# Optimization experiments

Hardware: AMD Instinct MI355X
Metric: run time of the kernel (lower is better)

## Reference

```python
import jax, jax.numpy as jnp
import numpy as np

NUM_PITCHES = 88
H_FEAT = 188
LSTM_UNITS = 48
N_STATES = 5
CTX_HID = 16
CTX_OUT = 4


def _glorot(key, shape):
    fan_in, fan_out = shape[1], shape[0]
    lim = (6.0 / (fan_in + fan_out)) ** 0.5
    return jax.random.uniform(key, shape, jnp.float32, -lim, lim)


def setup_inputs() -> dict:
    key = jax.random.key(0)
    ks = jax.random.split(key, 16)
    B, T = 16, 256
    pitch_features = jax.random.normal(ks[0], (B, NUM_PITCHES, H_FEAT, T), jnp.float32)
    prev_context = jax.random.uniform(ks[1], (B, NUM_PITCHES, 3), jnp.float32)
    # context net params
    fc1_w = _glorot(ks[2], (CTX_HID, 3)); fc1_b = jnp.zeros((CTX_HID,), jnp.float32)
    fc2_w = _glorot(ks[3], (CTX_HID, CTX_HID)); fc2_b = jnp.zeros((CTX_HID,), jnp.float32)
    fc3_w = _glorot(ks[4], (CTX_OUT, CTX_HID)); fc3_b = jnp.zeros((CTX_OUT,), jnp.float32)
    # lstm1: input H_FEAT+4 -> 48; gates order i,f,g,o (torch convention)
    in1 = H_FEAT + CTX_OUT
    lstm1_wih = _glorot(ks[5], (4 * LSTM_UNITS, in1))
    lstm1_whh = _glorot(ks[6], (4 * LSTM_UNITS, LSTM_UNITS))
    lstm1_bih = jnp.zeros((4 * LSTM_UNITS,), jnp.float32)
    lstm1_bhh = jnp.zeros((4 * LSTM_UNITS,), jnp.float32)
    lstm2_wih = _glorot(ks[7], (4 * LSTM_UNITS, LSTM_UNITS))
    lstm2_whh = _glorot(ks[8], (4 * LSTM_UNITS, LSTM_UNITS))
    lstm2_bih = jnp.zeros((4 * LSTM_UNITS,), jnp.float32)
    lstm2_bhh = jnp.zeros((4 * LSTM_UNITS,), jnp.float32)
    fc_states_w = _glorot(ks[9], (N_STATES, LSTM_UNITS))
    fc_states_b = jnp.zeros((N_STATES,), jnp.float32)
    return dict(pitch_features=pitch_features, prev_context=prev_context,
                fc1_w=fc1_w, fc1_b=fc1_b, fc2_w=fc2_w, fc2_b=fc2_b,
                fc3_w=fc3_w, fc3_b=fc3_b,
                lstm1_wih=lstm1_wih, lstm1_whh=lstm1_whh, lstm1_bih=lstm1_bih, lstm1_bhh=lstm1_bhh,
                lstm2_wih=lstm2_wih, lstm2_whh=lstm2_whh, lstm2_bih=lstm2_bih, lstm2_bhh=lstm2_bhh,
                fc_states_w=fc_states_w, fc_states_b=fc_states_b)


def _lstm_scan(x, wih, whh, bih, bhh):
    # x: (S, N, In); zero init state; returns (S, N, U)
    S, N, _ = x.shape
    U = whh.shape[1]
    xg = jnp.einsum('sni,gi->sng', x, wih) + bih + bhh  # precompute input gates

    def step(carry, xg_t):
        h, c = carry
        g = xg_t + h @ whh.T  # (N, 4U)
        i, f, gg, o = jnp.split(g, 4, axis=-1)
        c = jax.nn.sigmoid(f) * c + jax.nn.sigmoid(i) * jnp.tanh(gg)
        h = jax.nn.sigmoid(o) * jnp.tanh(c)
        return (h, c), h

    init = (jnp.zeros((N, U), x.dtype), jnp.zeros((N, U), x.dtype))
    _, hs = jax.lax.scan(step, init, xg)
    return hs


def reference(pitch_features, prev_context,
              fc1_w, fc1_b, fc2_w, fc2_b, fc3_w, fc3_b,
              lstm1_wih, lstm1_whh, lstm1_bih, lstm1_bhh,
              lstm2_wih, lstm2_whh, lstm2_bih, lstm2_bhh,
              fc_states_w, fc_states_b):
    B, P, H, T = pitch_features.shape
    # Context net (context never updates across t in the original loop)
    x = jax.nn.relu(prev_context @ fc1_w.T + fc1_b)
    x = jax.nn.relu(x @ fc2_w.T + fc2_b)
    ctx_emb = x @ fc3_w.T + fc3_b  # (B, P, 4)
    # Each timestep t is independent: LSTM runs over the pitch axis (len 88)
    # with zero initial state every step. Fold (B, T) into batch N.
    pf = jnp.transpose(pitch_features, (1, 0, 3, 2)).reshape(P, B * T, H)  # (P, BT, H)
    ce = jnp.broadcast_to(ctx_emb[:, None, :, :], (B, T, P, CTX_OUT))
    ce = jnp.transpose(ce, (2, 0, 1, 3)).reshape(P, B * T, CTX_OUT)
    seq = jnp.concatenate([pf, ce], axis=-1)  # (P, BT, H+4)
    h = _lstm_scan(seq, lstm1_wih, lstm1_whh, lstm1_bih, lstm1_bhh)
    h = _lstm_scan(h, lstm2_wih, lstm2_whh, lstm2_bih, lstm2_bhh)
    logits = h @ fc_states_w.T + fc_states_b  # (P, BT, 5)
    logits = logits.reshape(P, B, T, N_STATES)
    logits = jnp.transpose(logits, (1, 0, 3, 2))  # (B, P, 5, T)
    return jax.nn.softmax(logits, axis=2)
```

## Files before the change

### kernel.cpp

```cpp
#include <hip/hip_runtime.h>
#include <hip/hip_bf16.h>
#include <cstdint>

#define P_ 88
#define B_ 16
#define T_ 256
#define H_ 188
#define G_ 192
#define U_ 48
#define N_ 4096

typedef __attribute__((ext_vector_type(8))) short bf16x8;
typedef __attribute__((ext_vector_type(8))) _Float16 f16x8;
typedef __attribute__((ext_vector_type(4))) float f32x4;

__device__ __forceinline__ float sigf(float x) {
  return __builtin_amdgcn_rcpf(1.0f + __expf(-x));
}
__device__ __forceinline__ float tanh_f(float x) {
  return 1.0f - 2.0f * __builtin_amdgcn_rcpf(1.0f + __expf(2.0f * x));
}
__device__ __forceinline__ unsigned short f2bs(float v) {
  union { __hip_bfloat16 h; unsigned short s; } u;
  u.h = __float2bfloat16(v);
  return u.s;
}
__device__ __forceinline__ float bs2f(unsigned short s) {
  union { unsigned int u; float f; } x;
  x.u = ((unsigned int)s) << 16;
  return x.f;
}
__device__ __forceinline__ float hs2f(unsigned short s) {
  union { unsigned short u; _Float16 h; } x;
  x.u = s;
  return (float)x.h;
}
__device__ __forceinline__ unsigned short f2hs(float v) {
  union { _Float16 h; unsigned short s; } x;
  x.h = (_Float16)v;
  return x.s;
}

__device__ __forceinline__ void lds_barrier() {
  asm volatile("s_waitcnt lgkmcnt(0)\n\ts_barrier" ::: "memory");
}

__global__ void ctx_kernel(const float* __restrict__ pc,
                           const float* __restrict__ fc1w, const float* __restrict__ fc1b,
                           const float* __restrict__ fc2w, const float* __restrict__ fc2b,
                           const float* __restrict__ fc3w, const float* __restrict__ fc3b,
                           const float* __restrict__ wih1,
                           const float* __restrict__ bih1, const float* __restrict__ bhh1,
                           float* __restrict__ ctxg) {
  int bp = blockIdx.x * 64 + threadIdx.x;
  if (bp >= B_ * P_) return;
  float p0 = pc[bp * 3 + 0], p1 = pc[bp * 3 + 1], p2 = pc[bp * 3 + 2];
  float x1[16], x2[16];
#pragma unroll
  for (int jj = 0; jj < 16; ++jj)
    x1[jj] = fmaxf(0.f, fc1w[jj * 3 + 0] * p0 + fc1w[jj * 3 + 1] * p1 + fc1w[jj * 3 + 2] * p2 + fc1b[jj]);
#pragma unroll
  for (int jj = 0; jj < 16; ++jj) {
    float s = fc2b[jj];
#pragma unroll
    for (int i = 0; i < 16; ++i) s += fc2w[jj * 16 + i] * x1[i];
    x2[jj] = fmaxf(0.f, s);
  }
  float ce[4];
#pragma unroll
  for (int jj = 0; jj < 4; ++jj) {
    float s = fc3b[jj];
#pragma unroll
    for (int i = 0; i < 16; ++i) s += fc3w[jj * 16 + i] * x2[i];
    ce[jj] = s;
  }
  float* op = ctxg + (size_t)bp * G_;
  for (int g = 0; g < G_; ++g) {
    const float* wr = wih1 + (size_t)g * G_ + H_;
    op[g] = bih1[g] + bhh1[g] + ce[0] * wr[0] + ce[1] * wr[1] + ce[2] * wr[2] + ce[3] * wr[3];
  }
}

__global__ __launch_bounds__(256) void wfrag_kernel(const float* __restrict__ wih1,
                                                    f16x8* __restrict__ wfrag) {
  const int idx = blockIdx.x * 256 + threadIdx.x;
  if (idx >= 12 * 6 * 64) return;
  const int l = idx & 63;
  const int kc = (idx >> 6) % 6;
  const int j = idx / 384;
  const int g = j * 16 + (l & 15);
  const int k0 = kc * 32 + (l >> 4) * 8;
  f16x8 v;
#pragma unroll
  for (int e = 0; e < 8; ++e) {
    const int k = k0 + e;
    const float wv = (k < H_) ? wih1[(size_t)g * G_ + k] : 0.f;
    v[e] = (_Float16)wv;
  }
  wfrag[idx] = v;
}

__global__ __launch_bounds__(256, 3) void gemm_mfma(const float* __restrict__ pf,
                                                    const f16x8* __restrict__ wfrag,
                                                    const float* __restrict__ ctxg,
                                                    unsigned short* __restrict__ xg2) {
  const int bp = blockIdx.x >> 1, tb = blockIdx.x & 1;
  const int p = bp % P_, b = bp / P_;
  const int tid = threadIdx.x;
  const int w = tid >> 6, l = tid & 63;
  const int lj = l & 15, lq = l >> 4;

  __shared__ __align__(16) char ldsraw[49152];
  _Float16(*Ahi)[34] = (_Float16(*)[34])ldsraw;
  _Float16(*Alo)[34] = (_Float16(*)[34])(ldsraw + 8704);

  float cg[12];
#pragma unroll
  for (int jn = 0; jn < 12; ++jn)
    cg[jn] = ctxg[(size_t)bp * G_ + jn * 16 + lj];

  f32x4 acc[2][12];
#pragma unroll
  for (int mt = 0; mt < 2; ++mt)
#pragma unroll
    for (int jn = 0; jn < 12; ++jn)
#pragma unroll
      for (int r = 0; r < 4; ++r) acc[mt][jn][r] = 0.f;

  const float* Ab = pf + (size_t)bp * H_ * T_ + tb * 128;
  const int kl = tid >> 5;
  const int t4 = (tid & 31) * 4;

  for (int kc = 0; kc < 6; ++kc) {
    __syncthreads();
#pragma unroll
    for (int rr = 0; rr < 4; ++rr) {
      const int kk = rr * 8 + kl;
      const int kg = kc * 32 + kk;
      float a0 = 0.f, a1 = 0.f, a2 = 0.f, a3 = 0.f;
      if (kg < H_) {
        const float4 v = *(const float4*)(Ab + (size_t)kg * T_ + t4);
        a0 = v.x; a1 = v.y; a2 = v.z; a3 = v.w;
      }
      const _Float16 h0 = (_Float16)a0, h1 = (_Float16)a1;
      const _Float16 h2 = (_Float16)a2, h3 = (_Float16)a3;
      Ahi[t4 + 0][kk] = h0; Alo[t4 + 0][kk] = (_Float16)(a0 - (float)h0);
      Ahi[t4 + 1][kk] = h1; Alo[t4 + 1][kk] = (_Float16)(a1 - (float)h1);
      Ahi[t4 + 2][kk] = h2; Alo[t4 + 2][kk] = (_Float16)(a2 - (float)h2);
      Ahi[t4 + 3][kk] = h3; Alo[t4 + 3][kk] = (_Float16)(a3 - (float)h3);
    }
    __syncthreads();
    const int trow = w * 32;
    const f16x8 ahi0 = *(const f16x8*)&Ahi[trow + lj][lq * 8];
    const f16x8 ahi1 = *(const f16x8*)&Ahi[trow + 16 + lj][lq * 8];
    const f16x8 alo0 = *(const f16x8*)&Alo[trow + lj][lq * 8];
    const f16x8 alo1 = *(const f16x8*)&Alo[trow + 16 + lj][lq * 8];
#pragma unroll
    for (int jn = 0; jn < 12; ++jn) {
      const f16x8 wf = wfrag[(jn * 6 + kc) * 64 + l];
      acc[0][jn] = __builtin_amdgcn_mfma_f32_16x16x32_f16(ahi0, wf, acc[0][jn], 0, 0, 0);
      acc[1][jn] = __builtin_amdgcn_mfma_f32_16x16x32_f16(ahi1, wf, acc[1][jn], 0, 0, 0);
      acc[0][jn] = __builtin_amdgcn_mfma_f32_16x16x32_f16(alo0, wf, acc[0][jn], 0, 0, 0);
      acc[1][jn] = __builtin_amdgcn_mfma_f32_16x16x32_f16(alo1, wf, acc[1][jn], 0, 0, 0);
    }
  }
  __syncthreads();

  unsigned short* Cst = (unsigned short*)ldsraw + w * 6144;
#pragma unroll
  for (int mt = 0; mt < 2; ++mt)
#pragma unroll
    for (int jn = 0; jn < 12; ++jn)
#pragma unroll
      for (int r = 0; r < 4; ++r)
        Cst[mt * 3072 + jn * 256 + r * 64 + l] = f2hs(acc[mt][jn][r] + cg[jn]);
  const int nb0 = b * 16 + tb * 8 + w * 2;
  unsigned short* gb = xg2 + ((size_t)p * 256 + nb0) * 3072;
#pragma unroll
  for (int rr = 0; rr < 12; ++rr) {
    const uint4 v = *(const uint4*)(Cst + rr * 512 + l * 8);
    *(uint4*)(gb + rr * 512 + l * 8) = v;
  }
}

__global__ __launch_bounds__(256, 2) void scan_mfma(
    const unsigned short* __restrict__ xg2,
    const float* __restrict__ whh1, const float* __restrict__ wih2,
    const float* __restrict__ whh2, const float* __restrict__ bih2,
    const float* __restrict__ bhh2, const float* __restrict__ fcw,
    const float* __restrict__ fcb, float* __restrict__ out) {
  __shared__ __align__(16) short hh[16][104];
  __shared__ __align__(16) short hl[16][104];
  __shared__ __align__(16) float gs[8][196];
  __shared__ __align__(16) float h2f[8][52];
  __shared__ __align__(16) float fcws[5 * 48];
  __shared__ float logit_s[5][8];
  __shared__ float prob_s[5][8];

  const int tid = threadIdx.x;
  const int w = tid >> 6;
  const int l = tid & 63;
  const int lj = l & 15;
  const int lq = l >> 4;
  const int grp = blockIdx.x >> 1;
  const int half = blockIdx.x & 1;
  const int n0 = blockIdx.x * 8;
  const int b = n0 >> 8, t0 = n0 & 255;

  bf16x8 b1[3][2];
  bf16x8 b2f[3][3];
  float bias2r[3];
#pragma unroll
  for (int i = 0; i < 3; ++i) {
    const int j = w * 48 + i * 16 + lj;
    bias2r[i] = bih2[j] + bhh2[j];
#pragma unroll
    for (int kc = 0; kc < 2; ++kc)
#pragma unroll
      for (int e = 0; e < 8; ++e) {
        const int u = kc * 32 + lq * 8 + e;
        b1[i][kc][e] = (u < U_) ? (short)f2bs(whh1[j * U_ + u]) : (short)0;
      }
#pragma unroll
    for (int kc = 0; kc < 3; ++kc)
#pragma unroll
      for (int e = 0; e < 8; ++e) {
        const int u = kc * 32 + lq * 8 + e;
        b2f[i][kc][e] = (u < U_) ? (short)f2bs(wih2[j * U_ + u])
                                 : (short)f2bs(whh2[j * U_ + (u - U_)]);
      }
  }

  for (int e = tid; e < 16 * 104 / 2; e += 256) {
    ((unsigned int*)hh)[e] = 0u;
    ((unsigned int*)hl)[e] = 0u;
  }
  for (int e = tid; e < 5 * U_; e += 256) fcws[e] = fcw[e];

  const int tn0 = tid / U_, tu0 = tid % U_;
  const int tn1 = (256 + tid) / U_, tu1 = (256 + tid) % U_;
  float c1r[2] = {0.f, 0.f}, c2r[2] = {0.f, 0.f};
  const bool fcth = tid < 40;
  const int fk = tid >> 3, fn = tid & 7;
  const float fcbr = fcth ? fcb[fk] : 0.f;
  const int sk = (tid - 96) >> 3, sn = (tid - 96) & 7;

  unsigned short xp[12];
  {
    const size_t pb = (size_t)grp * 3072;
#pragma unroll
    for (int i = 0; i < 3; ++i)
#pragma unroll
      for (int r = 0; r < 4; ++r)
        xp[i * 4 + r] = (lq < 2)
            ? xg2[pb + (size_t)((w * 3 + i) * 256 + r * 64 + (half * 2 + lq) * 16 + lj)]
            : (unsigned short)0;
  }
  const short* hhrow = &hh[lj][0];
  const short* hlrow = &hl[lj][0];
  lds_barrier();

  for (int p = 0; p < P_; ++p) {
    f32x4 cH[3], cL[3];
#pragma unroll
    for (int i = 0; i < 3; ++i)
#pragma unroll
      for (int r = 0; r < 4; ++r) { cH[i][r] = hs2f(xp[i * 4 + r]); cL[i][r] = 0.f; }
    if (p < P_ - 1) {
      const size_t pb = (size_t)((p + 1) * 256 + grp) * 3072;
#pragma unroll
      for (int i = 0; i < 3; ++i)
#pragma unroll
        for (int r = 0; r < 4; ++r)
          xp[i * 4 + r] = (lq < 2)
              ? xg2[pb + (size_t)((w * 3 + i) * 256 + r * 64 + (half * 2 + lq) * 16 + lj)]
              : (unsigned short)0;
    }
    {
      bf16x8 ah0 = *(const bf16x8*)(hhrow + lq * 8);
      bf16x8 ah1 = *(const bf16x8*)(hhrow + 32 + lq * 8);
      bf16x8 al0 = *(const bf16x8*)(hlrow + lq * 8);
      bf16x8 al1 = *(const bf16x8*)(hlrow + 32 + lq * 8);
#pragma unroll
      for (int i = 0; i < 3; ++i)
        cH[i] = __builtin_amdgcn_mfma_f32_16x16x32_bf16(ah0, b1[i][0], cH[i], 0, 0, 0);
#pragma unroll
      for (int i = 0; i < 3; ++i)
        cL[i] = __builtin_amdgcn_mfma_f32_16x16x32_bf16(al0, b1[i][0], cL[i], 0, 0, 0);
#pragma unroll
      for (int i = 0; i < 3; ++i)
        cH[i] = __builtin_amdgcn_mfma_f32_16x16x32_bf16(ah1, b1[i][1], cH[i], 0, 0, 0);
#pragma unroll
      for (int i = 0; i < 3; ++i)
        cL[i] = __builtin_amdgcn_mfma_f32_16x16x32_bf16(al1, b1[i][1], cL[i], 0, 0, 0);
    }
    if (lq < 2) {
#pragma unroll
      for (int i = 0; i < 3; ++i)
#pragma unroll
        for (int r = 0; r < 4; ++r)
          gs[lq * 4 + r][w * 48 + i * 16 + lj] = cH[i][r] + cL[i][r];
    }
    if (p > 0 && fcth) {
      float a = fcbr;
#pragma unroll
      for (int uq = 0; uq < 12; ++uq) {
        f32x4 hv = *(const f32x4*)&h2f[fn][uq * 4];
        f32x4 wv = *(const f32x4*)&fcws[fk * 48 + uq * 4];
        a += hv[0] * wv[0] + hv[1] * wv[1] + hv[2] * wv[2] + hv[3] * wv[3];
      }
      logit_s[fk][fn] = a;
    }
    lds_barrier();
    {
      const int n = tn0, u = tu0;
      const float ig = gs[n][u], fg = gs[n][48 + u];
      const float gg = gs[n][96 + u], og = gs[n][144 + u];
      const float cc = sigf(fg) * c1r[0] + sigf(ig) * tanh_f(gg);
      c1r[0] = cc;
      const float h = sigf(og) * tanh_f(cc);
      const unsigned short hb = f2bs(h);
      hh[n][u] = (short)hb;
      hl[n][u] = (short)f2bs(h - bs2f(hb));
    }
    if (tid < 128) {
      const int n = tn1, u = tu1;
      const float ig = gs[n][u], fg = gs[n][48 + u];
      const float gg = gs[n][96 + u], og = gs[n][144 + u];
      const float cc = sigf(fg) * c1r[1] + sigf(ig) * tanh_f(gg);
      c1r[1] = cc;
      const float h = sigf(og) * tanh_f(cc);
      const unsigned short hb = f2bs(h);
      hh[n][u] = (short)hb;
      hl[n][u] = (short)f2bs(h - bs2f(hb));
    }
    if (p > 0 && tid >= 192 && tid < 200) {
      const int n = tid - 192;
      const float l0 = logit_s[0][n], l1 = logit_s[1][n], l2 = logit_s[2][n],
                  l3 = logit_s[3][n], l4 = logit_s[4][n];
      const float m = fmaxf(fmaxf(fmaxf(l0, l1), fmaxf(l2, l3)), l4);
      const float e0 = __expf(l0 - m), e1 = __expf(l1 - m), e2 = __expf(l2 - m),
                  e3 = __expf(l3 - m), e4 = __expf(l4 - m);
      const float rs = __builtin_amdgcn_rcpf(e0 + e1 + e2 + e3 + e4);
      prob_s[0][n] = e0 * rs; prob_s[1][n] = e1 * rs; prob_s[2][n] = e2 * rs;
      prob_s[3][n] = e3 * rs; prob_s[4][n] = e4 * rs;
    }
    lds_barrier();
    f32x4 c2H[3], c2L[3];
#pragma unroll
    for (int i = 0; i < 3; ++i) {
      c2H[i][0] = bias2r[i]; c2H[i][1] = bias2r[i];
      c2H[i][2] = bias2r[i]; c2H[i][3] = bias2r[i];
      c2L[i][0] = 0.f; c2L[i][1] = 0.f; c2L[i][2] = 0.f; c2L[i][3] = 0.f;
    }
    {
      bf16x8 a0 = *(const bf16x8*)(hhrow + lq * 8);
      bf16x8 a1 = *(const bf16x8*)(hhrow + 32 + lq * 8);
      bf16x8 a2 = *(const bf16x8*)(hhrow + 64 + lq * 8);
      bf16x8 q0 = *(const bf16x8*)(hlrow + lq * 8);
      bf16x8 q1 = *(const bf16x8*)(hlrow + 32 + lq * 8);
      bf16x8 q2 = *(const bf16x8*)(hlrow + 64 + lq * 8);
#pragma unroll
      for (int i = 0; i < 3; ++i)
        c2H[i] = __builtin_amdgcn_mfma_f32_16x16x32_bf16(a0, b2f[i][0], c2H[i], 0, 0, 0);
#pragma unroll
      for (int i = 0; i < 3; ++i)
        c2L[i] = __builtin_amdgcn_mfma_f32_16x16x32_bf16(q0, b2f[i][0], c2L[i], 0, 0, 0);
#pragma unroll
      for (int i = 0; i < 3; ++i)
        c2H[i] = __builtin_amdgcn_mfma_f32_16x16x32_bf16(a1, b2f[i][1], c2H[i], 0, 0, 0);
#pragma unroll
      for (int i = 0; i < 3; ++i)
        c2L[i] = __builtin_amdgcn_mfma_f32_16x16x32_bf16(q1, b2f[i][1], c2L[i], 0, 0, 0);
#pragma unroll
      for (int i = 0; i < 3; ++i)
        c2H[i] = __builtin_amdgcn_mfma_f32_16x16x32_bf16(a2, b2f[i][2], c2H[i], 0, 0, 0);
#pragma unroll
      for (int i = 0; i < 3; ++i)
        c2L[i] = __builtin_amdgcn_mfma_f32_16x16x32_bf16(q2, b2f[i][2], c2L[i], 0, 0, 0);
    }
    if (lq < 2) {
#pragma unroll
      for (int i = 0; i < 3; ++i)
#pragma unroll
        for (int r = 0; r < 4; ++r)
          gs[lq * 4 + r][w * 48 + i * 16 + lj] = c2H[i][r] + c2L[i][r];
    }
    if (p > 0 && tid >= 96 && tid < 136) {
      out[(((size_t)b * P_ + (p - 1)) * 5 + sk) * T_ + t0 + sn] = prob_s[sk][sn];
    }
    lds_barrier();
    {
      const int n = tn0, u = tu0;
      const float ig = gs[n][u], fg = gs[n][48 + u];
      const float gg = gs[n][96 + u], og = gs[n][144 + u];
      const float cc = sigf(fg) * c2r[0] + sigf(ig) * tanh_f(gg);
      c2r[0] = cc;
      const float h = sigf(og) * tanh_f(cc);
      const unsigned short hb = f2bs(h);
      hh[n][48 + u] = (short)hb;
      hl[n][48 + u] = (short)f2bs(h - bs2f(hb));
      h2f[n][u] = h;
    }
    if (tid < 128) {
      const int n = tn1, u = tu1;
      const float ig = gs[n][u], fg = gs[n][48 + u];
      const float gg = gs[n][96 + u], og = gs[n][144 + u];
      const float cc = sigf(fg) * c2r[1] + sigf(ig) * tanh_f(gg);
      c2r[1] = cc;
      const float h = sigf(og) * tanh_f(cc);
      const unsigned short hb = f2bs(h);
      hh[n][48 + u] = (short)hb;
      hl[n][48 + u] = (short)f2bs(h - bs2f(hb));
      h2f[n][u] = h;
    }
    lds_barrier();
  }
  if (fcth) {
    float a = fcbr;
#pragma unroll
    for (int uq = 0; uq < 12; ++uq) {
      f32x4 hv = *(const f32x4*)&h2f[fn][uq * 4];
      f32x4 wv = *(const f32x4*)&fcws[fk * 48 + uq * 4];
      a += hv[0] * wv[0] + hv[1] * wv[1] + hv[2] * wv[2] + hv[3] * wv[3];
    }
    logit_s[fk][fn] = a;
  }
  lds_barrier();
  if (tid >= 192 && tid < 200) {
    const int n = tid - 192;
    const float l0 = logit_s[0][n], l1 = logit_s[1][n], l2 = logit_s[2][n],
                l3 = logit_s[3][n], l4 = logit_s[4][n];
    const float m = fmaxf(fmaxf(fmaxf(l0, l1), fmaxf(l2, l3)), l4);
    const float e0 = __expf(l0 - m), e1 = __expf(l1 - m), e2 = __expf(l2 - m),
                e3 = __expf(l3 - m), e4 = __expf(l4 - m);
    const float rs = __builtin_amdgcn_rcpf(e0 + e1 + e2 + e3 + e4);
    prob_s[0][n] = e0 * rs; prob_s[1][n] = e1 * rs; prob_s[2][n] = e2 * rs;
    prob_s[3][n] = e3 * rs; prob_s[4][n] = e4 * rs;
  }
  lds_barrier();
  if (tid >= 96 && tid < 136) {
    out[(((size_t)b * P_ + (P_ - 1)) * 5 + sk) * T_ + t0 + sn] = prob_s[sk][sn];
  }
}

extern "C" void kernel_launch(void* const* d_in, const int* in_sizes, int n_in,
                              void* d_out, int out_size, void* d_ws, size_t ws_size,
                              hipStream_t stream) {
  const float* pf   = (const float*)d_in[0];
  const float* pc   = (const float*)d_in[1];
  const float* fc1w = (const float*)d_in[2];
  const float* fc1b = (const float*)d_in[3];
  const float* fc2w = (const float*)d_in[4];
  const float* fc2b = (const float*)d_in[5];
  const float* fc3w = (const float*)d_in[6];
  const float* fc3b = (const float*)d_in[7];
  const float* wih1 = (const float*)d_in[8];
  const float* whh1 = (const float*)d_in[9];
  const float* bih1 = (const float*)d_in[10];
  const float* bhh1 = (const float*)d_in[11];
  const float* wih2 = (const float*)d_in[12];
  const float* whh2 = (const float*)d_in[13];
  const float* bih2 = (const float*)d_in[14];
  const float* bhh2 = (const float*)d_in[15];
  const float* fcw  = (const float*)d_in[16];
  const float* fcb  = (const float*)d_in[17];
  float* out = (float*)d_out;

  char* wsp = (char*)d_ws;
  float* ctxg = (float*)wsp;
  const size_t CTXG_BYTES = (size_t)B_ * P_ * G_ * sizeof(float);
  f16x8* wfrag = (f16x8*)(wsp + CTXG_BYTES);
  const size_t WFRAG_BYTES = (size_t)12 * 6 * 64 * 16;
  unsigned short* xg2 = (unsigned short*)(wsp + CTXG_BYTES + WFRAG_BYTES);

  ctx_kernel<<<22, 64, 0, stream>>>(pc, fc1w, fc1b, fc2w, fc2b, fc3w, fc3b,
                                    wih1, bih1, bhh1, ctxg);
  wfrag_kernel<<<18, 256, 0, stream>>>(wih1, wfrag);
  gemm_mfma<<<B_ * P_ * 2, 256, 0, stream>>>(pf, wfrag, ctxg, xg2);
  scan_mfma<<<N_ / 8, 256, 0, stream>>>(xg2, whh1, wih2, whh2,
                                        bih2, bhh2, fcw, fcb, out);
}
```

Baseline: 413.2 us.

## Permute gate columns so each wave owns its units, halving block barriers

The input-gate precompute kernel now stores gate columns in a permuted order, so each wave's MFMA output tile holds all four gates for its own 12 hidden units. The cell update can then read gates from a per-wave LDS buffer after a wave-local lgkmcnt wait, with no block barrier. The h state is double-buffered across pitch steps, so each step needs two block barriers instead of four. The softmax and output-store work is re-staggered by one more step, and the hi/lo bf16 split now truncates instead of rounding.

```diff
diff --git a/kernel.cpp b/kernel.cpp
--- a/kernel.cpp
+++ b/kernel.cpp
@@ -40,9 +40,29 @@
   x.h = (_Float16)v;
   return x.s;
 }
+__device__ __forceinline__ void hsplit(float h, unsigned short& hi, unsigned short& lo) {
+  union { float f; unsigned int u; } x;
+  x.f = h;
+  hi = (unsigned short)(x.u >> 16);
+  union { float f; unsigned int u; } y;
+  y.f = h - bs2f(hi);
+  lo = (unsigned short)(y.u >> 16);
+}
 
 __device__ __forceinline__ void lds_barrier() {
   asm volatile("s_waitcnt lgkmcnt(0)\n\ts_barrier" ::: "memory");
+}
+__device__ __forceinline__ void lds_wave_fence() {
+  asm volatile("s_waitcnt lgkmcnt(0)" ::: "memory");
+}
+
+__device__ __forceinline__ int scan_slot(int g) {
+  const int t = g / 48;
+  const int u = g - t * 48;
+  const int ws = u / 12;
+  const int ul = u - ws * 12;
+  const int c = t * 12 + ul;
+  return (ws * 3 + (c >> 4)) * 256 + (c & 15);
 }
 
 __global__ void ctx_kernel(const float* __restrict__ pc,
@@ -170,10 +190,12 @@
 #pragma unroll
   for (int mt = 0; mt < 2; ++mt)
 #pragma unroll
-    for (int jn = 0; jn < 12; ++jn)
+    for (int jn = 0; jn < 12; ++jn) {
+      const int sbase = scan_slot(jn * 16 + lj) + lq * 16;
 #pragma unroll
       for (int r = 0; r < 4; ++r)
-        Cst[mt * 3072 + jn * 256 + r * 64 + l] = f2hs(acc[mt][jn][r] + cg[jn]);
+        Cst[mt * 3072 + sbase + r * 64] = f2hs(acc[mt][jn][r] + cg[jn]);
+    }
   const int nb0 = b * 16 + tb * 8 + w * 2;
   unsigned short* gb = xg2 + ((size_t)p * 256 + nb0) * 3072;
 #pragma unroll
@@ -189,9 +211,9 @@
     const float* __restrict__ whh2, const float* __restrict__ bih2,
     const float* __restrict__ bhh2, const float* __restrict__ fcw,
     const float* __restrict__ fcb, float* __restrict__ out) {
-  __shared__ __align__(16) short hh[16][104];
-  __shared__ __align__(16) short hl[16][104];
-  __shared__ __align__(16) float gs[8][196];
+  __shared__ __align__(16) short hh[2][16][104];
+  __shared__ __align__(16) short hl[2][16][104];
+  __shared__ __align__(16) float gsw[4][8][52];
   __shared__ __align__(16) float h2f[8][52];
   __shared__ __align__(16) float fcws[5 * 48];
   __shared__ float logit_s[5][8];
@@ -212,7 +234,9 @@
   float bias2r[3];
 #pragma unroll
   for (int i = 0; i < 3; ++i) {
-    const int j = w * 48 + i * 16 + lj;
+    const int c = i * 16 + lj;
+    const int t = c / 12, ul = c - t * 12;
+    const int j = t * 48 + w * 12 + ul;
     bias2r[i] = bih2[j] + bhh2[j];
 #pragma unroll
     for (int kc = 0; kc < 2; ++kc)
@@ -225,25 +249,33 @@
     for (int kc = 0; kc < 3; ++kc)
 #pragma unroll
       for (int e = 0; e < 8; ++e) {
-        const int u = kc * 32 + lq * 8 + e;
-        b2f[i][kc][e] = (u < U_) ? (short)f2bs(wih2[j * U_ + u])
-                                 : (short)f2bs(whh2[j * U_ + (u - U_)]);
+        const int k = kc * 32 + lq * 8 + e;
+        b2f[i][kc][e] = (k < U_) ? (short)f2bs(wih2[j * U_ + k])
+                                 : (short)f2bs(whh2[j * U_ + (k - U_)]);
       }
   }
 
-  for (int e = tid; e < 16 * 104 / 2; e += 256) {
+  for (int e = tid; e < 2 * 16 * 104 / 2; e += 256) {
     ((unsigned int*)hh)[e] = 0u;
     ((unsigned int*)hl)[e] = 0u;
   }
   for (int e = tid; e < 5 * U_; e += 256) fcws[e] = fcw[e];
 
-  const int tn0 = tid / U_, tu0 = tid % U_;
-  const int tn1 = (256 + tid) / U_, tu1 = (256 + tid) % U_;
-  float c1r[2] = {0.f, 0.f}, c2r[2] = {0.f, 0.f};
-  const bool fcth = tid < 40;
-  const int fk = tid >> 3, fn = tid & 7;
+  const int an0 = l / 12, au0 = l - an0 * 12;
+  const int an1 = (64 + l) / 12, au1 = (64 + l) - an1 * 12;
+  const int aug0 = w * 12 + au0, aug1 = w * 12 + au1;
+  const bool has2 = (l < 32);
+  float c1s[2] = {0.f, 0.f}, c2s[2] = {0.f, 0.f};
+
+  const bool fcth = (l < 10);
+  const int tf = w * 10 + l;
+  const int fk = tf >> 3, fn = tf & 7;
   const float fcbr = fcth ? fcb[fk] : 0.f;
-  const int sk = (tid - 96) >> 3, sn = (tid - 96) & 7;
+  const bool stth = (l >= 10 && l < 20);
+  const int ts = w * 10 + (l - 10);
+  const int sk = ts >> 3, sn = ts & 7;
+  const bool smth = (l >= 20 && l < 22);
+  const int sm = w * 2 + (l - 20);
 
   unsigned short xp[12];
   {
@@ -256,11 +288,10 @@
             ? xg2[pb + (size_t)((w * 3 + i) * 256 + r * 64 + (half * 2 + lq) * 16 + lj)]
             : (unsigned short)0;
   }
-  const short* hhrow = &hh[lj][0];
-  const short* hlrow = &hl[lj][0];
   lds_barrier();
 
   for (int p = 0; p < P_; ++p) {
+    const int cur = p & 1, alt = cur ^ 1;
     f32x4 cH[3], cL[3];
 #pragma unroll
     for (int i = 0; i < 3; ++i)
@@ -277,10 +308,12 @@
               : (unsigned short)0;
     }
     {
-      bf16x8 ah0 = *(const bf16x8*)(hhrow + lq * 8);
-      bf16x8 ah1 = *(const bf16x8*)(hhrow + 32 + lq * 8);
-      bf16x8 al0 = *(const bf16x8*)(hlrow + lq * 8);
-      bf16x8 al1 = *(const bf16x8*)(hlrow + 32 + lq * 8);
+      const short* hr = &hh[alt][lj][0];
+      const short* lr = &hl[alt][lj][0];
+      bf16x8 ah0 = *(const bf16x8*)(hr + lq * 8);
+      bf16x8 ah1 = *(const bf16x8*)(hr + 32 + lq * 8);
+      bf16x8 al0 = *(const bf16x8*)(lr + lq * 8);
+      bf16x8 al1 = *(const bf16x8*)(lr + 32 + lq * 8);
 #pragma unroll
       for (int i = 0; i < 3; ++i)
         cH[i] = __builtin_amdgcn_mfma_f32_16x16x32_bf16(ah0, b1[i][0], cH[i], 0, 0, 0);
@@ -299,7 +332,7 @@
       for (int i = 0; i < 3; ++i)
 #pragma unroll
         for (int r = 0; r < 4; ++r)
-          gs[lq * 4 + r][w * 48 + i * 16 + lj] = cH[i][r] + cL[i][r];
+          gsw[w][lq * 4 + r][i * 16 + lj] = cH[i][r] + cL[i][r];
     }
     if (p > 0 && fcth) {
       float a = fcbr;
@@ -311,31 +344,77 @@
       }
       logit_s[fk][fn] = a;
     }
+    if (p > 1 && stth) {
+      out[(((size_t)b * P_ + (p - 2)) * 5 + sk) * T_ + t0 + sn] = prob_s[sk][sn];
+    }
+    lds_wave_fence();
+    {
+      const float ig = gsw[w][an0][au0],      fg = gsw[w][an0][12 + au0];
+      const float gg = gsw[w][an0][24 + au0], og = gsw[w][an0][36 + au0];
+      const float cc = sigf(fg) * c1s[0] + sigf(ig) * tanh_f(gg);
+      c1s[0] = cc;
+      const float h = sigf(og) * tanh_f(cc);
+      unsigned short hb, lb;
+      hsplit(h, hb, lb);
+      hh[cur][an0][aug0] = (short)hb;
+      hl[cur][an0][aug0] = (short)lb;
+    }
+    if (has2) {
+      const float ig = gsw[w][an1][au1],      fg = gsw[w][an1][12 + au1];
+      const float gg = gsw[w][an1][24 + au1], og = gsw[w][an1][36 + au1];
+      const float cc = sigf(fg) * c1s[1] + sigf(ig) * tanh_f(gg);
+      c1s[1] = cc;
+      const float h = sigf(og) * tanh_f(cc);
+      unsigned short hb, lb;
+      hsplit(h, hb, lb);
+      hh[cur][an1][aug1] = (short)hb;
+      hl[cur][an1][aug1] = (short)lb;
+    }
     lds_barrier();
+    f32x4 c2H[3], c2L[3];
+#pragma unroll
+    for (int i = 0; i < 3; ++i) {
+      c2H[i][0] = bias2r[i]; c2H[i][1] = bias2r[i];
+      c2H[i][2] = bias2r[i]; c2H[i][3] = bias2r[i];
+      c2L[i][0] = 0.f; c2L[i][1] = 0.f; c2L[i][2] = 0.f; c2L[i][3] = 0.f;
+    }
     {
-      const int n = tn0, u = tu0;
-      const float ig = gs[n][u], fg = gs[n][48 + u];
-      const float gg = gs[n][96 + u], og = gs[n][144 + u];
-      const float cc = sigf(fg) * c1r[0] + sigf(ig) * tanh_f(gg);
-      c1r[0] = cc;
-      const float h = sigf(og) * tanh_f(cc);
-      const unsigned short hb = f2bs(h);
-      hh[n][u] = (short)hb;
-      hl[n][u] = (short)f2bs(h - bs2f(hb));
-    }
-    if (tid < 128) {
-      const int n = tn1, u = tu1;
-      const float ig = gs[n][u], fg = gs[n][48 + u];
-      const float gg = gs[n][96 + u], og = gs[n][144 + u];
-      const float cc = sigf(fg) * c1r[1] + sigf(ig) * tanh_f(gg);
-      c1r[1] = cc;
-      const float h = sigf(og) * tanh_f(cc);
-      const unsigned short hb = f2bs(h);
-      hh[n][u] = (short)hb;
-      hl[n][u] = (short)f2bs(h - bs2f(hb));
-    }
-    if (p > 0 && tid >= 192 && tid < 200) {
-      const int n = tid - 192;
+      const short* hr = &hh[cur][lj][0];
+      const short* lr = &hl[cur][lj][0];
+      bf16x8 a0 = *(const bf16x8*)(hr + lq * 8);
+      bf16x8 a1 = *(const bf16x8*)(hr + 32 + lq * 8);
+      bf16x8 a2 = *(const bf16x8*)(hr + 64 + lq * 8);
+      bf16x8 q0 = *(const bf16x8*)(lr + lq * 8);
+      bf16x8 q1 = *(const bf16x8*)(lr + 32 + lq * 8);
+      bf16x8 q2 = *(const bf16x8*)(lr + 64 + lq * 8);
+#pragma unroll
+      for (int i = 0; i < 3; ++i)
+        c2H[i] = __builtin_amdgcn_mfma_f32_16x16x32_bf16(a0, b2f[i][0], c2H[i], 0, 0, 0);
+#pragma unroll
+      for (int i = 0; i < 3; ++i)
+        c2L[i] = __builtin_amdgcn_mfma_f32_16x16x32_bf16(q0, b2f[i][0], c2L[i], 0, 0, 0);
+#pragma unroll
+      for (int i = 0; i < 3; ++i)
+        c2H[i] = __builtin_amdgcn_mfma_f32_16x16x32_bf16(a1, b2f[i][1], c2H[i], 0, 0, 0);
+#pragma unroll
+      for (int i = 0; i < 3; ++i)
+        c2L[i] = __builtin_amdgcn_mfma_f32_16x16x32_bf16(q1, b2f[i][1], c2L[i], 0, 0, 0);
+#pragma unroll
+      for (int i = 0; i < 3; ++i)
+        c2H[i] = __builtin_amdgcn_mfma_f32_16x16x32_bf16(a2, b2f[i][2], c2H[i], 0, 0, 0);
+#pragma unroll
+      for (int i = 0; i < 3; ++i)
+        c2L[i] = __builtin_amdgcn_mfma_f32_16x16x32_bf16(q2, b2f[i][2], c2L[i], 0, 0, 0);
+    }
+    if (lq < 2) {
+#pragma unroll
+      for (int i = 0; i < 3; ++i)
+#pragma unroll
+        for (int r = 0; r < 4; ++r)
+          gsw[w][lq * 4 + r][i * 16 + lj] = c2H[i][r] + c2L[i][r];
+    }
+    if (p > 0 && smth) {
+      const int n = sm;
       const float l0 = logit_s[0][n], l1 = logit_s[1][n], l2 = logit_s[2][n],
                   l3 = logit_s[3][n], l4 = logit_s[4][n];
       const float m = fmaxf(fmaxf(fmaxf(l0, l1), fmaxf(l2, l3)), l4);
@@ -345,74 +424,30 @@
       prob_s[0][n] = e0 * rs; prob_s[1][n] = e1 * rs; prob_s[2][n] = e2 * rs;
       prob_s[3][n] = e3 * rs; prob_s[4][n] = e4 * rs;
     }
-    lds_barrier();
-    f32x4 c2H[3], c2L[3];
-#pragma unroll
-    for (int i = 0; i < 3; ++i) {
-      c2H[i][0] = bias2r[i]; c2H[i][1] = bias2r[i];
-      c2H[i][2] = bias2r[i]; c2H[i][3] = bias2r[i];
-      c2L[i][0] = 0.f; c2L[i][1] = 0.f; c2L[i][2] = 0.f; c2L[i][3] = 0.f;
-    }
+    lds_wave_fence();
     {
-      bf16x8 a0 = *(const bf16x8*)(hhrow + lq * 8);
-      bf16x8 a1 = *(const bf16x8*)(hhrow + 32 + lq * 8);
-      bf16x8 a2 = *(const bf16x8*)(hhrow + 64 + lq * 8);
-      bf16x8 q0 = *(const bf16x8*)(hlrow + lq * 8);
-      bf16x8 q1 = *(const bf16x8*)(hlrow + 32 + lq * 8);
-      bf16x8 q2 = *(const bf16x8*)(hlrow + 64 + lq * 8);
-#pragma unroll
-      for (int i = 0; i < 3; ++i)
-        c2H[i] = __builtin_amdgcn_mfma_f32_16x16x32_bf16(a0, b2f[i][0], c2H[i], 0, 0, 0);
-#pragma unroll
-      for (int i = 0; i < 3; ++i)
-        c2L[i] = __builtin_amdgcn_mfma_f32_16x16x32_bf16(q0, b2f[i][0], c2L[i], 0, 0, 0);
-#pragma unroll
-      for (int i = 0; i < 3; ++i)
-        c2H[i] = __builtin_amdgcn_mfma_f32_16x16x32_bf16(a1, b2f[i][1], c2H[i], 0, 0, 0);
-#pragma unroll
-      for (int i = 0; i < 3; ++i)
-        c2L[i] = __builtin_amdgcn_mfma_f32_16x16x32_bf16(q1, b2f[i][1], c2L[i], 0, 0, 0);
-#pragma unroll
-      for (int i = 0; i < 3; ++i)
-        c2H[i] = __builtin_amdgcn_mfma_f32_16x16x32_bf16(a2, b2f[i][2], c2H[i], 0, 0, 0);
-#pragma unroll
-      for (int i = 0; i < 3; ++i)
-        c2L[i] = __builtin_amdgcn_mfma_f32_16x16x32_bf16(q2, b2f[i][2], c2L[i], 0, 0, 0);
-    }
-    if (lq < 2) {
-#pragma unroll
-      for (int i = 0; i < 3; ++i)
-#pragma unroll
-        for (int r = 0; r < 4; ++r)
-          gs[lq * 4 + r][w * 48 + i * 16 + lj] = c2H[i][r] + c2L[i][r];
-    }
-    if (p > 0 && tid >= 96 && tid < 136) {
-      out[(((size_t)b * P_ + (p - 1)) * 5 + sk) * T_ + t0 + sn] = prob_s[sk][sn];
-    }
-    lds_barrier();
-    {
-      const int n = tn0, u = tu0;
-      const float ig = gs[n][u], fg = gs[n][48 + u];
-      const float gg = gs[n][96 + u], og = gs[n][144 + u];
-      const float cc = sigf(fg) * c2r[0] + sigf(ig) * tanh_f(gg);
-      c2r[0] = cc;
+      const float ig = gsw[w][an0][au0],      fg = gsw[w][an0][12 + au0];
+      const float gg = gsw[w][an0][24 + au0], og = gsw[w][an0][36 + au0];
+      const float cc = sigf(fg) * c2s[0] + sigf(ig) * tanh_f(gg);
+      c2s[0] = cc;
       const float h = sigf(og) * tanh_f(cc);
-      const unsigned short hb = f2bs(h);
-      hh[n][48 + u] = (short)hb;
-      hl[n][48 + u] = (short)f2bs(h - bs2f(hb));
-      h2f[n][u] = h;
-    }
-    if (tid < 128) {
-      const int n = tn1, u = tu1;
-      const float ig = gs[n][u], fg = gs[n][48 + u];
-      const float gg = gs[n][96 + u], og = gs[n][144 + u];
-      const float cc = sigf(fg) * c2r[1] + sigf(ig) * tanh_f(gg);
-      c2r[1] = cc;
+      unsigned short hb, lb;
+      hsplit(h, hb, lb);
+      hh[alt][an0][48 + aug0] = (short)hb;
+      hl[alt][an0][48 + aug0] = (short)lb;
+      h2f[an0][aug0] = h;
+    }
+    if (has2) {
+      const float ig = gsw[w][an1][au1],      fg = gsw[w][an1][12 + au1];
+      const float gg = gsw[w][an1][24 + au1], og = gsw[w][an1][36 + au1];
+      const float cc = sigf(fg) * c2s[1] + sigf(ig) * tanh_f(gg);
+      c2s[1] = cc;
       const float h = sigf(og) * tanh_f(cc);
-      const unsigned short hb = f2bs(h);
-      hh[n][48 + u] = (short)hb;
-      hl[n][48 + u] = (short)f2bs(h - bs2f(hb));
-      h2f[n][u] = h;
+      unsigned short hb, lb;
+      hsplit(h, hb, lb);
+      hh[alt][an1][48 + aug1] = (short)hb;
+      hl[alt][an1][48 + aug1] = (short)lb;
+      h2f[an1][aug1] = h;
     }
     lds_barrier();
   }
@@ -426,9 +461,12 @@
     }
     logit_s[fk][fn] = a;
   }
+  if (stth) {
+    out[(((size_t)b * P_ + (P_ - 2)) * 5 + sk) * T_ + t0 + sn] = prob_s[sk][sn];
+  }
   lds_barrier();
-  if (tid >= 192 && tid < 200) {
-    const int n = tid - 192;
+  if (smth) {
+    const int n = sm;
     const float l0 = logit_s[0][n], l1 = logit_s[1][n], l2 = logit_s[2][n],
                 l3 = logit_s[3][n], l4 = logit_s[4][n];
     const float m = fmaxf(fmaxf(fmaxf(l0, l1), fmaxf(l2, l3)), l4);
@@ -439,7 +477,7 @@
     prob_s[3][n] = e3 * rs; prob_s[4][n] = e4 * rs;
   }
   lds_barrier();
-  if (tid >= 96 && tid < 136) {
+  if (stth) {
     out[(((size_t)b * P_ + (P_ - 1)) * 5 + sk) * T_ + t0 + sn] = prob_s[sk][sn];
   }
 }
```

After: 454.9 us. 10.1% more time.
